# Performance work log

Hardware: AMD Instinct MI355X
Metric: run time of the kernel (lower is better)

## Reference

```python
import jax, jax.numpy as jnp
import numpy as np

D_IN = 1024
D_OUT = 1024


def setup_inputs() -> dict:
    key = jax.random.key(0)
    kx, kq, kk, kv = jax.random.split(key, 4)
    x = jax.random.normal(kx, (4, 2048, D_IN), dtype=jnp.float32)
    # nn.Linear weight has shape [d_out, d_in]; y = x @ W.T
    s = 1.0 / np.sqrt(D_IN)
    W_query = jax.random.uniform(kq, (D_OUT, D_IN), jnp.float32, -s, s)
    W_key = jax.random.uniform(kk, (D_OUT, D_IN), jnp.float32, -s, s)
    W_value = jax.random.uniform(kv, (D_OUT, D_IN), jnp.float32, -s, s)
    return {"x": x, "W_query": W_query, "W_key": W_key, "W_value": W_value}


def reference(x, W_query, W_key, W_value):
    # x: [b, n, d_in]; W_*: [d_out, d_in]
    q = jnp.einsum("bnd,kd->bnk", x, W_query)
    k = jnp.einsum("bnd,kd->bnk", x, W_key)
    v = jnp.einsum("bnd,kd->bnk", x, W_value)
    d_k = W_query.shape[0]
    scores = jnp.einsum("bqk,bnk->bqn", q, k) * (d_k ** -0.5)  # [b, n, n]
    weights = jax.nn.softmax(scores, axis=-1)
    return jnp.einsum("bqn,bnk->bqk", weights, v)
```

## Files before the change

### kernel.cpp

```cpp
#include <hip/hip_runtime.h>
#include <hip/hip_bf16.h>
#include <stdint.h>


typedef __attribute__((ext_vector_type(8))) short bf16x8;
typedef __attribute__((ext_vector_type(4))) float f32x4;

__device__ __forceinline__ void async_copy16(const void* g, void* l) {
  __builtin_amdgcn_global_load_lds(
      (__attribute__((address_space(1))) void*)(g),
      (__attribute__((address_space(3))) void*)(l),
      16, 0, 0);
}

__device__ __forceinline__ void mainloop256(
    const __hip_bfloat16* __restrict__ aS,
    const __hip_bfloat16* __restrict__ bS,
    __hip_bfloat16* As, __hip_bfloat16* Bs,
    const int wid, const int wm, const int wn,
    const int l16, const int quad, const int sw,
    f32x4 (&acc)[8][4])
{
  const bf16x8* Av = (const bf16x8*)As;
  const bf16x8* Bv = (const bf16x8*)Bs;
  char* lA = (char*)As + wid * 1024;
  char* lB = (char*)Bs + wid * 1024;
  bf16x8 bfr[4][2];

#define STG_A(t, h) do { \
    async_copy16(aS + (((h)*128 +  0) * 1024 + (t)*64), lA + ((t)&1)*32768 + ((h)*128 +  0)*128); \
    async_copy16(aS + (((h)*128 + 64) * 1024 + (t)*64), lA + ((t)&1)*32768 + ((h)*128 + 64)*128); \
  } while (0)
#define STG_B(t, h) do { \
    async_copy16(bS + (((h)*128 +  0) * 1024 + (t)*64), lB + ((t)&1)*32768 + ((h)*128 +  0)*128); \
    async_copy16(bS + (((h)*128 + 64) * 1024 + (t)*64), lB + ((t)&1)*32768 + ((h)*128 + 64)*128); \
  } while (0)

#define PH(t, phi, LOADB, STAGE_STMT, TAIL_STMT) do { \
    bf16x8 af[2][2]; \
    const int bofs = ((t)&1) * 2048;   \
    _Pragma("unroll") \
    for (int m2 = 0; m2 < 2; ++m2) \
      _Pragma("unroll") \
      for (int kk = 0; kk < 2; ++kk) \
        af[m2][kk] = Av[bofs + (wm + ((phi)*2 + m2)*16 + l16)*8 + ((kk*4 + quad) ^ sw)]; \
    if (LOADB) { \
      _Pragma("unroll") \
      for (int ni = 0; ni < 4; ++ni) \
        _Pragma("unroll") \
        for (int kk = 0; kk < 2; ++kk) \
          bfr[ni][kk] = Bv[bofs + (wn + ni*16 + l16)*8 + ((kk*4 + quad) ^ sw)]; \
    } \
    STAGE_STMT; \
    __builtin_amdgcn_sched_barrier(0); \
    __builtin_amdgcn_s_barrier(); \
    asm volatile("s_waitcnt lgkmcnt(0)"); \
    __builtin_amdgcn_sched_barrier(0); \
    __builtin_amdgcn_s_setprio(1); \
    _Pragma("unroll") \
    for (int kk = 0; kk < 2; ++kk) \
      _Pragma("unroll") \
      for (int m2 = 0; m2 < 2; ++m2) \
        _Pragma("unroll") \
        for (int ni = 0; ni < 4; ++ni) \
          acc[(phi)*2 + m2][ni] = __builtin_amdgcn_mfma_f32_16x16x32_bf16( \
              af[m2][kk], bfr[ni][kk], acc[(phi)*2 + m2][ni], 0, 0, 0); \
    __builtin_amdgcn_s_setprio(0); \
    TAIL_STMT; \
    __builtin_amdgcn_sched_barrier(0); \
    __builtin_amdgcn_s_barrier(); \
  } while (0)

  STG_B(0, 0); STG_B(0, 1); STG_A(0, 0); STG_A(0, 1); STG_B(1, 0); STG_B(1, 1);
  asm volatile("s_waitcnt vmcnt(4)");
  __builtin_amdgcn_s_barrier();

  #pragma unroll 1
  for (int i = 0; i < 7; ++i) {
    const int ta = 2 * i, tb = 2 * i + 1;
    PH(ta, 0, true,  STG_A(tb, 0),     (void)0);
    PH(ta, 1, false, STG_A(tb, 1),     (void)0);
    PH(ta, 2, false, STG_B(ta + 2, 0), (void)0);
    PH(ta, 3, false, STG_B(ta + 2, 1), asm volatile("s_waitcnt vmcnt(4)"));
    PH(tb, 0, true,  STG_A(ta + 2, 0), (void)0);
    PH(tb, 1, false, STG_A(ta + 2, 1), (void)0);
    PH(tb, 2, false, STG_B(tb + 2, 0), (void)0);
    PH(tb, 3, false, STG_B(tb + 2, 1), asm volatile("s_waitcnt vmcnt(4)"));
  }
  PH(14, 0, true,  STG_A(15, 0), (void)0);
  PH(14, 1, false, STG_A(15, 1), (void)0);
  PH(14, 2, false, (void)0,      (void)0);
  PH(14, 3, false, (void)0,      asm volatile("s_waitcnt vmcnt(0)"));
  PH(15, 0, true,  (void)0, (void)0);
  PH(15, 1, false, (void)0, (void)0);
  PH(15, 2, false, (void)0, (void)0);
  PH(15, 3, false, (void)0, (void)0);

#undef PH
#undef STG_A
#undef STG_B
}

__global__ __launch_bounds__(512, 2)
void gemm_qkv(const __hip_bfloat16* __restrict__ A,
              const __hip_bfloat16* __restrict__ B,
              __hip_bfloat16* __restrict__ Q,
              __hip_bfloat16* __restrict__ Kk,
              __hip_bfloat16* __restrict__ Vt)
{
  __shared__ __align__(16) __hip_bfloat16 As[2][256 * 64];
  __shared__ __align__(16) __hip_bfloat16 Bs[2][256 * 64];

  const int bid = blockIdx.x;
  const int s   = (bid & 7) * 48 + (bid >> 3);
  const long long tile_m = (long long)(s / 12) * 256;
  const long long tile_n = (long long)(s % 12) * 256;

  const int tid  = threadIdx.x;
  const int wid  = tid >> 6;
  const int lane = tid & 63;
  const int srow = wid * 8 + (lane >> 3);
  const int scol = ((lane & 7) ^ (lane >> 3)) * 8;

  const __hip_bfloat16* aS = A + (tile_m + srow) * 1024 + scol;
  const __hip_bfloat16* bS = B + (tile_n + srow) * 1024 + scol;

  const int wm   = (wid >> 2) * 128;
  const int wn   = (wid & 3) * 64;
  const int quad = lane >> 4;
  const int l16  = lane & 15;
  const int sw   = l16 & 7;

  f32x4 acc[8][4];
  #pragma unroll
  for (int mi = 0; mi < 8; ++mi)
    #pragma unroll
    for (int ni = 0; ni < 4; ++ni)
      acc[mi][ni] = (f32x4){0.f, 0.f, 0.f, 0.f};

  mainloop256(aS, bS, &As[0][0], &Bs[0][0], wid, wm, wn, l16, quad, sw, acc);

  const int mat = (int)(tile_n >> 10);
  if (mat < 2) {
    __hip_bfloat16* outp = (mat == 0) ? Q : Kk;
    const float scale = (mat == 0) ? 0.03125f : 1.0f;
    const int coln0 = (int)(tile_n & 1023);
    #pragma unroll
    for (int mi = 0; mi < 8; ++mi) {
      #pragma unroll
      for (int r = 0; r < 4; ++r) {
        const long long row = tile_m + wm + mi * 16 + quad * 4 + r;
        #pragma unroll
        for (int ni = 0; ni < 4; ++ni) {
          const int col = coln0 + wn + ni * 16 + l16;
          outp[row * 1024 + col] = __float2bfloat16(acc[mi][ni][r] * scale);
        }
      }
    }
  } else {
    const int b    = (int)(tile_m >> 11);
    const int seq0 = (int)(tile_m & 2047);
    const int d0   = (int)(tile_n - 2048);
    #pragma unroll
    for (int mi = 0; mi < 8; ++mi) {
      const int seq = seq0 + wm + mi * 16 + quad * 4;
      #pragma unroll
      for (int ni = 0; ni < 4; ++ni) {
        const int d = d0 + wn + ni * 16 + l16;
        union { ushort4 u; unsigned short sh[4]; } pk;
        #pragma unroll
        for (int r = 0; r < 4; ++r)
          pk.sh[r] = __bfloat16_as_ushort(__float2bfloat16(acc[mi][ni][r]));
        *(ushort4*)(Vt + ((long long)(b * 1024 + d)) * 2048 + seq) = pk.u;
      }
    }
  }
}

__global__ __launch_bounds__(512, 2)
void gemm_s_exp(const __hip_bfloat16* __restrict__ A,
                const __hip_bfloat16* __restrict__ B,
                __hip_bfloat16* __restrict__ Cout,
                float* __restrict__ part)
{
  __shared__ __align__(16) __hip_bfloat16 As[2][256 * 64];
  __shared__ __align__(16) __hip_bfloat16 Bs[2][256 * 64];

  const int bz = blockIdx.z;
  A += (long long)bz * 2048 * 1024;
  B += (long long)bz * 2048 * 1024;

  const long long tile_m = (long long)blockIdx.y * 256;
  const long long tile_n = (long long)blockIdx.x * 256;

  const int tid  = threadIdx.x;
  const int wid  = tid >> 6;
  const int lane = tid & 63;
  const int srow = wid * 8 + (lane >> 3);
  const int scol = ((lane & 7) ^ (lane >> 3)) * 8;

  const __hip_bfloat16* aS = A + (tile_m + srow) * 1024 + scol;
  const __hip_bfloat16* bS = B + (tile_n + srow) * 1024 + scol;

  const int wm   = (wid >> 2) * 128;
  const int wn   = (wid & 3) * 64;
  const int quad = lane >> 4;
  const int l16  = lane & 15;
  const int sw   = l16 & 7;

  f32x4 acc[8][4];
  #pragma unroll
  for (int mi = 0; mi < 8; ++mi)
    #pragma unroll
    for (int ni = 0; ni < 4; ++ni)
      acc[mi][ni] = (f32x4){0.f, 0.f, 0.f, 0.f};

  mainloop256(aS, bS, &As[0][0], &Bs[0][0], wid, wm, wn, l16, quad, sw, acc);

  __hip_bfloat16* C = Cout + (long long)bz * 2048 * 2048;
  #pragma unroll
  for (int mi = 0; mi < 8; ++mi) {
    #pragma unroll
    for (int r = 0; r < 4; ++r) {
      const long long row = tile_m + wm + mi * 16 + quad * 4 + r;
      float ssum = 0.f;
      #pragma unroll
      for (int ni = 0; ni < 4; ++ni) {
        const float e = __expf(acc[mi][ni][r]);
        const __hip_bfloat16 h = __float2bfloat16(e);
        C[row * 2048 + tile_n + wn + ni * 16 + l16] = h;
        ssum += __bfloat162float(h);
      }
      #pragma unroll
      for (int off = 1; off < 16; off <<= 1) ssum += __shfl_xor(ssum, off, 64);
      if (l16 == 0)
        part[((long long)bz * 2048 + row) * 32 + blockIdx.x * 4 + (wid & 3)] = ssum;
    }
  }
}

__global__ __launch_bounds__(256)
void gemm_pv(const __hip_bfloat16* __restrict__ A,
             const __hip_bfloat16* __restrict__ B,
             const float* __restrict__ part,
             float* __restrict__ Cout)
{
  __shared__ __align__(16) __hip_bfloat16 As[128 * 64];
  __shared__ __align__(16) __hip_bfloat16 Bs[64 * 64];
  __shared__ float rinv[128];

  const int K = 2048, N = 1024;
  const int bz = blockIdx.z;
  A += (long long)bz * 2048 * 2048;
  B += (long long)bz * 1024 * 2048;

  const long long tile_m = (long long)blockIdx.y * 128;
  const long long tile_n = (long long)blockIdx.x * 64;

  const int tid  = threadIdx.x;
  const int wid  = tid >> 6;
  const int lane = tid & 63;

  const int srow = wid * 8 + (lane >> 3);
  const int scol = (((lane & 7) ^ (lane >> 3))) * 8;

  const __hip_bfloat16* aptr = A + (tile_m + srow) * K + scol;
  const __hip_bfloat16* bptr = B + (tile_n + srow) * K + scol;
  char* la = (char*)As + (wid * 8) * 128;
  char* lb = (char*)Bs + (wid * 8) * 128;

  const int wm   = (wid >> 1) * 64;
  const int wn   = (wid & 1) * 32;
  const int quad = lane >> 4;
  const int l16  = lane & 15;
  const int sw   = l16 & 7;

  const bf16x8* Asv = (const bf16x8*)As;
  const bf16x8* Bsv = (const bf16x8*)Bs;

  f32x4 acc[4][2];
  #pragma unroll
  for (int mi = 0; mi < 4; ++mi)
    #pragma unroll
    for (int ni = 0; ni < 2; ++ni)
      acc[mi][ni] = (f32x4){0.f, 0.f, 0.f, 0.f};

  for (int k0 = 0; k0 < K; k0 += 64) {
    #pragma unroll
    for (int p = 0; p < 4; ++p)
      async_copy16(aptr + (long long)p * 32 * K, la + p * 32 * 128);
    #pragma unroll
    for (int p = 0; p < 2; ++p)
      async_copy16(bptr + (long long)p * 32 * K, lb + p * 32 * 128);
    aptr += 64;
    bptr += 64;
    __syncthreads();

    #pragma unroll
    for (int kk = 0; kk < 2; ++kk) {
      bf16x8 af[4], bfr[2];
      const int ch = (kk * 4 + quad);
      #pragma unroll
      for (int mi = 0; mi < 4; ++mi) af[mi]  = Asv[(wm + mi * 16 + l16) * 8 + (ch ^ sw)];
      #pragma unroll
      for (int ni = 0; ni < 2; ++ni) bfr[ni] = Bsv[(wn + ni * 16 + l16) * 8 + (ch ^ sw)];
      #pragma unroll
      for (int mi = 0; mi < 4; ++mi)
        #pragma unroll
        for (int ni = 0; ni < 2; ++ni)
          acc[mi][ni] = __builtin_amdgcn_mfma_f32_16x16x32_bf16(af[mi], bfr[ni], acc[mi][ni], 0, 0, 0);
    }
    __syncthreads();
  }

  if (tid < 128) {
    const float4* pp = (const float4*)(part + ((long long)bz * 2048 + tile_m + tid) * 32);
    float s = 0.f;
    #pragma unroll
    for (int j = 0; j < 8; ++j) {
      const float4 f = pp[j];
      s += f.x + f.y + f.z + f.w;
    }
    rinv[tid] = 1.f / s;
  }
  __syncthreads();

  float* C = Cout + (long long)bz * 2048 * 1024;
  #pragma unroll
  for (int mi = 0; mi < 4; ++mi) {
    #pragma unroll
    for (int r = 0; r < 4; ++r) {
      const int rloc = wm + mi * 16 + quad * 4 + r;
      const float inv = rinv[rloc];
      const long long row = tile_m + rloc;
      #pragma unroll
      for (int ni = 0; ni < 2; ++ni) {
        const long long col = tile_n + wn + ni * 16 + l16;
        C[row * N + col] = acc[mi][ni][r] * inv;
      }
    }
  }
}

__global__ __launch_bounds__(256)
void cast_all(const float* __restrict__ x,
              const float* __restrict__ Wq, const float* __restrict__ Wk,
              const float* __restrict__ Wv,
              __hip_bfloat16* __restrict__ xb, __hip_bfloat16* __restrict__ wcat)
{
  const int bx = blockIdx.x;
  const float* src;
  __hip_bfloat16* dst;
  int i;
  if (bx < 8192) {
    src = x; dst = xb; i = bx * 256 + threadIdx.x;
  } else {
    const int which = (bx - 8192) >> 10;
    src = (which == 0) ? Wq : (which == 1) ? Wk : Wv;
    dst = wcat + (long long)which * 1048576;
    i = ((bx - 8192) & 1023) * 256 + threadIdx.x;
  }
  const float4 f = ((const float4*)src)[i];
  union { ushort4 u; __hip_bfloat16 h[4]; } r;
  r.h[0] = __float2bfloat16(f.x);
  r.h[1] = __float2bfloat16(f.y);
  r.h[2] = __float2bfloat16(f.z);
  r.h[3] = __float2bfloat16(f.w);
  ((ushort4*)dst)[i] = r.u;
}

extern "C" void kernel_launch(void* const* d_in, const int* in_sizes, int n_in,
                              void* d_out, int out_size, void* d_ws, size_t ws_size,
                              hipStream_t stream)
{
  (void)in_sizes; (void)n_in; (void)out_size; (void)ws_size;

  const float* x  = (const float*)d_in[0];
  const float* Wq = (const float*)d_in[1];
  const float* Wk = (const float*)d_in[2];
  const float* Wv = (const float*)d_in[3];
  float* out = (float*)d_out;

  char* ws = (char*)d_ws;
  __hip_bfloat16* xb   = (__hip_bfloat16*)(ws);
  float*          part = (float*)(ws);
  __hip_bfloat16* wcat = (__hip_bfloat16*)(ws + (16LL << 20));
  __hip_bfloat16* Q    = (__hip_bfloat16*)(ws + (22LL << 20));
  __hip_bfloat16* Kk   = (__hip_bfloat16*)(ws + (38LL << 20));
  __hip_bfloat16* Vt   = (__hip_bfloat16*)(ws + (54LL << 20));
  __hip_bfloat16* S    = (__hip_bfloat16*)(ws + (70LL << 20));

  cast_all<<<11264, 256, 0, stream>>>(x, Wq, Wk, Wv, xb, wcat);

  gemm_qkv<<<dim3(384, 1, 1), 512, 0, stream>>>(xb, wcat, Q, Kk, Vt);

  gemm_s_exp<<<dim3(8, 8, 4), 512, 0, stream>>>(Q, Kk, S, part);

  gemm_pv<<<dim3(16, 16, 4), 256, 0, stream>>>(S, Vt, part, out);
}
```

Baseline: 246.8 us.

## Restructure QKV GEMM mainloop per k-tile and widen PV GEMM tile to 128x128

```diff
diff --git a/kernel.cpp b/kernel.cpp
--- a/kernel.cpp
+++ b/kernel.cpp
@@ -26,79 +26,109 @@
   char* lA = (char*)As + wid * 1024;
   char* lB = (char*)Bs + wid * 1024;
   bf16x8 bfr[4][2];
-
-#define STG_A(t, h) do { \
-    async_copy16(aS + (((h)*128 +  0) * 1024 + (t)*64), lA + ((t)&1)*32768 + ((h)*128 +  0)*128); \
-    async_copy16(aS + (((h)*128 + 64) * 1024 + (t)*64), lA + ((t)&1)*32768 + ((h)*128 + 64)*128); \
-  } while (0)
-#define STG_B(t, h) do { \
-    async_copy16(bS + (((h)*128 +  0) * 1024 + (t)*64), lB + ((t)&1)*32768 + ((h)*128 +  0)*128); \
-    async_copy16(bS + (((h)*128 + 64) * 1024 + (t)*64), lB + ((t)&1)*32768 + ((h)*128 + 64)*128); \
-  } while (0)
-
-#define PH(t, phi, LOADB, STAGE_STMT, TAIL_STMT) do { \
-    bf16x8 af[2][2]; \
-    const int bofs = ((t)&1) * 2048;   \
+  bf16x8 afc[2][2], afn[2][2];
+
+#define SB0 __builtin_amdgcn_sched_barrier(0)
+
+#define STG_A2(t) do { \
+    async_copy16(aS + ((t)*64 +        0), lA + ((t)&1)*32768 +        0); \
+    async_copy16(aS + ((t)*64 +  64*1024), lA + ((t)&1)*32768 +  64*128); \
+    async_copy16(aS + ((t)*64 + 128*1024), lA + ((t)&1)*32768 + 128*128); \
+    async_copy16(aS + ((t)*64 + 192*1024), lA + ((t)&1)*32768 + 192*128); \
+  } while (0)
+#define STG_B2(t) do { \
+    async_copy16(bS + ((t)*64 +        0), lB + ((t)&1)*32768 +        0); \
+    async_copy16(bS + ((t)*64 +  64*1024), lB + ((t)&1)*32768 +  64*128); \
+    async_copy16(bS + ((t)*64 + 128*1024), lB + ((t)&1)*32768 + 128*128); \
+    async_copy16(bS + ((t)*64 + 192*1024), lB + ((t)&1)*32768 + 192*128); \
+  } while (0)
+
+#define RD_AF(dst, t, phi) do { \
     _Pragma("unroll") \
     for (int m2 = 0; m2 < 2; ++m2) \
       _Pragma("unroll") \
       for (int kk = 0; kk < 2; ++kk) \
-        af[m2][kk] = Av[bofs + (wm + ((phi)*2 + m2)*16 + l16)*8 + ((kk*4 + quad) ^ sw)]; \
-    if (LOADB) { \
+        dst[m2][kk] = Av[((t)&1)*2048 + (wm + ((phi)*2 + m2)*16 + l16)*8 + ((kk*4 + quad) ^ sw)]; \
+  } while (0)
+#define RD_BF(t, nlo, nhi) do { \
+    _Pragma("unroll") \
+    for (int ni = (nlo); ni < (nhi); ++ni) \
       _Pragma("unroll") \
-      for (int ni = 0; ni < 4; ++ni) \
-        _Pragma("unroll") \
-        for (int kk = 0; kk < 2; ++kk) \
-          bfr[ni][kk] = Bv[bofs + (wn + ni*16 + l16)*8 + ((kk*4 + quad) ^ sw)]; \
-    } \
-    STAGE_STMT; \
-    __builtin_amdgcn_sched_barrier(0); \
-    __builtin_amdgcn_s_barrier(); \
-    asm volatile("s_waitcnt lgkmcnt(0)"); \
-    __builtin_amdgcn_sched_barrier(0); \
-    __builtin_amdgcn_s_setprio(1); \
+      for (int kk = 0; kk < 2; ++kk) \
+        bfr[ni][kk] = Bv[((t)&1)*2048 + (wn + ni*16 + l16)*8 + ((kk*4 + quad) ^ sw)]; \
+  } while (0)
+#define MM(src, phi, nlo, nhi) do { \
     _Pragma("unroll") \
     for (int kk = 0; kk < 2; ++kk) \
       _Pragma("unroll") \
       for (int m2 = 0; m2 < 2; ++m2) \
         _Pragma("unroll") \
-        for (int ni = 0; ni < 4; ++ni) \
+        for (int ni = (nlo); ni < (nhi); ++ni) \
           acc[(phi)*2 + m2][ni] = __builtin_amdgcn_mfma_f32_16x16x32_bf16( \
-              af[m2][kk], bfr[ni][kk], acc[(phi)*2 + m2][ni], 0, 0, 0); \
-    __builtin_amdgcn_s_setprio(0); \
-    TAIL_STMT; \
-    __builtin_amdgcn_sched_barrier(0); \
+              src[m2][kk], bfr[ni][kk], acc[(phi)*2 + m2][ni], 0, 0, 0); \
+  } while (0)
+
+#define TILE(t, STG0_STMT, STG1_STMT, GATE_STMT) do { \
+     \
+    RD_BF(t, 0, 2); \
+    RD_AF(afc, t, 0); \
+    STG0_STMT; \
+    asm volatile("s_waitcnt lgkmcnt(0)"); SB0; \
+    RD_BF(t, 2, 4); \
+    SB0; \
+    RD_AF(afn, t, 1); \
+    SB0; \
+    __builtin_amdgcn_s_setprio(1); MM(afc, 0, 0, 2); __builtin_amdgcn_s_setprio(0); \
+    asm volatile("s_waitcnt lgkmcnt(4)"); SB0; \
+    __builtin_amdgcn_s_setprio(1); MM(afc, 0, 2, 4); __builtin_amdgcn_s_setprio(0); \
+    SB0; \
+    __builtin_amdgcn_s_barrier();    \
+     \
+    STG1_STMT; \
+    asm volatile("s_waitcnt lgkmcnt(0)"); SB0; \
+    RD_AF(afc, t, 2); \
+    SB0; \
+    __builtin_amdgcn_s_setprio(1); MM(afn, 1, 0, 4); __builtin_amdgcn_s_setprio(0); \
+     \
+    asm volatile("s_waitcnt lgkmcnt(0)"); SB0; \
+    RD_AF(afn, t, 3); \
+    SB0; \
+    __builtin_amdgcn_s_setprio(1); MM(afc, 2, 0, 4); __builtin_amdgcn_s_setprio(0); \
+     \
+    asm volatile("s_waitcnt lgkmcnt(0)"); SB0; \
+    __builtin_amdgcn_s_setprio(1); MM(afn, 3, 0, 4); __builtin_amdgcn_s_setprio(0); \
+    GATE_STMT; \
+    SB0; \
     __builtin_amdgcn_s_barrier(); \
   } while (0)
 
-  STG_B(0, 0); STG_B(0, 1); STG_A(0, 0); STG_A(0, 1); STG_B(1, 0); STG_B(1, 1);
+#define GATE4 asm volatile("s_waitcnt vmcnt(4)")
+#define GATE0 asm volatile("s_waitcnt vmcnt(0)")
+#define GNONE (void)0
+
+  STG_B2(0); STG_A2(0); STG_B2(1);
   asm volatile("s_waitcnt vmcnt(4)");
   __builtin_amdgcn_s_barrier();
 
   #pragma unroll 1
   for (int i = 0; i < 7; ++i) {
     const int ta = 2 * i, tb = 2 * i + 1;
-    PH(ta, 0, true,  STG_A(tb, 0),     (void)0);
-    PH(ta, 1, false, STG_A(tb, 1),     (void)0);
-    PH(ta, 2, false, STG_B(ta + 2, 0), (void)0);
-    PH(ta, 3, false, STG_B(ta + 2, 1), asm volatile("s_waitcnt vmcnt(4)"));
-    PH(tb, 0, true,  STG_A(ta + 2, 0), (void)0);
-    PH(tb, 1, false, STG_A(ta + 2, 1), (void)0);
-    PH(tb, 2, false, STG_B(tb + 2, 0), (void)0);
-    PH(tb, 3, false, STG_B(tb + 2, 1), asm volatile("s_waitcnt vmcnt(4)"));
-  }
-  PH(14, 0, true,  STG_A(15, 0), (void)0);
-  PH(14, 1, false, STG_A(15, 1), (void)0);
-  PH(14, 2, false, (void)0,      (void)0);
-  PH(14, 3, false, (void)0,      asm volatile("s_waitcnt vmcnt(0)"));
-  PH(15, 0, true,  (void)0, (void)0);
-  PH(15, 1, false, (void)0, (void)0);
-  PH(15, 2, false, (void)0, (void)0);
-  PH(15, 3, false, (void)0, (void)0);
-
-#undef PH
-#undef STG_A
-#undef STG_B
+    TILE(ta, STG_A2(tb),     STG_B2(ta + 2), GATE4);
+    TILE(tb, STG_A2(ta + 2), STG_B2(tb + 2), GATE4);
+  }
+  TILE(14, STG_A2(15), GNONE, GATE0);
+  TILE(15, GNONE,      GNONE, GNONE);
+
+#undef TILE
+#undef GATE4
+#undef GATE0
+#undef GNONE
+#undef MM
+#undef RD_BF
+#undef RD_AF
+#undef STG_A2
+#undef STG_B2
+#undef SB0
 }
 
 __global__ __launch_bounds__(512, 2)
@@ -246,7 +276,7 @@
              float* __restrict__ Cout)
 {
   __shared__ __align__(16) __hip_bfloat16 As[128 * 64];
-  __shared__ __align__(16) __hip_bfloat16 Bs[64 * 64];
+  __shared__ __align__(16) __hip_bfloat16 Bs[128 * 64];
   __shared__ float rinv[128];
 
   const int K = 2048, N = 1024;
@@ -255,7 +285,7 @@
   B += (long long)bz * 1024 * 2048;
 
   const long long tile_m = (long long)blockIdx.y * 128;
-  const long long tile_n = (long long)blockIdx.x * 64;
+  const long long tile_n = (long long)blockIdx.x * 128;
 
   const int tid  = threadIdx.x;
   const int wid  = tid >> 6;
@@ -270,7 +300,7 @@
   char* lb = (char*)Bs + (wid * 8) * 128;
 
   const int wm   = (wid >> 1) * 64;
-  const int wn   = (wid & 1) * 32;
+  const int wn   = (wid & 1) * 64;
   const int quad = lane >> 4;
   const int l16  = lane & 15;
   const int sw   = l16 & 7;
@@ -278,11 +308,11 @@
   const bf16x8* Asv = (const bf16x8*)As;
   const bf16x8* Bsv = (const bf16x8*)Bs;
 
-  f32x4 acc[4][2];
+  f32x4 acc[4][4];
   #pragma unroll
   for (int mi = 0; mi < 4; ++mi)
     #pragma unroll
-    for (int ni = 0; ni < 2; ++ni)
+    for (int ni = 0; ni < 4; ++ni)
       acc[mi][ni] = (f32x4){0.f, 0.f, 0.f, 0.f};
 
   for (int k0 = 0; k0 < K; k0 += 64) {
@@ -290,7 +320,7 @@
     for (int p = 0; p < 4; ++p)
       async_copy16(aptr + (long long)p * 32 * K, la + p * 32 * 128);
     #pragma unroll
-    for (int p = 0; p < 2; ++p)
+    for (int p = 0; p < 4; ++p)
       async_copy16(bptr + (long long)p * 32 * K, lb + p * 32 * 128);
     aptr += 64;
     bptr += 64;
@@ -298,16 +328,16 @@
 
     #pragma unroll
     for (int kk = 0; kk < 2; ++kk) {
-      bf16x8 af[4], bfr[2];
+      bf16x8 af[4], bfr[4];
       const int ch = (kk * 4 + quad);
       #pragma unroll
       for (int mi = 0; mi < 4; ++mi) af[mi]  = Asv[(wm + mi * 16 + l16) * 8 + (ch ^ sw)];
       #pragma unroll
-      for (int ni = 0; ni < 2; ++ni) bfr[ni] = Bsv[(wn + ni * 16 + l16) * 8 + (ch ^ sw)];
+      for (int ni = 0; ni < 4; ++ni) bfr[ni] = Bsv[(wn + ni * 16 + l16) * 8 + (ch ^ sw)];
       #pragma unroll
       for (int mi = 0; mi < 4; ++mi)
         #pragma unroll
-        for (int ni = 0; ni < 2; ++ni)
+        for (int ni = 0; ni < 4; ++ni)
           acc[mi][ni] = __builtin_amdgcn_mfma_f32_16x16x32_bf16(af[mi], bfr[ni], acc[mi][ni], 0, 0, 0);
     }
     __syncthreads();
@@ -334,7 +364,7 @@
       const float inv = rinv[rloc];
       const long long row = tile_m + rloc;
       #pragma unroll
-      for (int ni = 0; ni < 2; ++ni) {
+      for (int ni = 0; ni < 4; ++ni) {
         const long long col = tile_n + wn + ni * 16 + l16;
         C[row * N + col] = acc[mi][ni][r] * inv;
       }
@@ -396,5 +426,5 @@
 
   gemm_s_exp<<<dim3(8, 8, 4), 512, 0, stream>>>(Q, Kk, S, part);
 
-  gemm_pv<<<dim3(16, 16, 4), 256, 0, stream>>>(S, Vt, part, out);
-}
+  gemm_pv<<<dim3(8, 16, 4), 256, 0, stream>>>(S, Vt, part, out);
+}
```

Result: faster. 236.4 us (-4.2%).
